# Kernel optimization log

Measured on AMD Instinct MI355X. Metric: run time of the kernel, lower is better.

The kernel has to match this reference:

```python
import jax, jax.numpy as jnp
import numpy as np

NUM_EXPERT = 8
IN_FEAT = 512
OUT_FEAT = 512
TOKENS = 16384


def setup_inputs() -> dict:
    key = jax.random.key(0)
    k_inp, k_gate, k_w = jax.random.split(key, 3)
    inp = jax.random.uniform(k_inp, (TOKENS, IN_FEAT), dtype=jnp.float32)
    gate = jax.random.randint(k_gate, (TOKENS,), 0, NUM_EXPERT, dtype=jnp.int32)
    # nn.Linear-style init: U(-1/sqrt(in_feat), 1/sqrt(in_feat))
    bound = 1.0 / np.sqrt(IN_FEAT)
    weight = jax.random.uniform(
        k_w, (NUM_EXPERT, OUT_FEAT, IN_FEAT), dtype=jnp.float32,
        minval=-bound, maxval=bound)
    return {"inp": inp, "gate": gate, "weight": weight}


def reference(inp, gate, weight):
    # y_t = weight[gate[t]] @ x_t  (per-token expert-specific GEMM)
    # Implemented via one-hot dispatch to avoid gathering a [T, O, I] weight tensor.
    num_expert = weight.shape[0]
    dispatch = jax.nn.one_hot(gate, num_expert, dtype=inp.dtype)  # [T, E]
    xe = jnp.einsum('te,ti->eti', dispatch, inp)                  # [E, T, I]
    ye = jnp.einsum('eti,eoi->eto', xe, weight)                   # [E, T, O]
    out = jnp.einsum('eto,te->to', ye, dispatch)                  # [T, O]
    return out
```

## Files before the change

kernel.cpp:

```cpp
#include <hip/hip_runtime.h>
#include <hip/hip_bf16.h>

#define TOKENS 16384
#define NEXP 8
#define INF 512
#define OUTF 512

#define BM 64
#define BN 128
#define BK 64
#define NST (INF / BK)
#define MAXMT 40
#define EROWS (MAXMT * BM)

using f32x4 = __attribute__((ext_vector_type(4))) float;
using bfrag = __attribute__((ext_vector_type(8))) __bf16;
using s8v   = __attribute__((ext_vector_type(8))) short;

__device__ __forceinline__ short f2bf(float f) {
  union { float f; unsigned u; } v; v.f = f;
  unsigned r = v.u + 0x7fffu + ((v.u >> 16) & 1u);
  return (short)(r >> 16);
}

__device__ __forceinline__ void gload16(const void* g, void* l) {
  __builtin_amdgcn_global_load_lds(
      (const __attribute__((address_space(1))) unsigned int*)g,
      (__attribute__((address_space(3))) unsigned int*)l, 16, 0, 0);
}

__device__ __forceinline__ s8v pack8(float4 a, float4 b) {
  s8v p;
  p[0] = f2bf(a.x); p[1] = f2bf(a.y); p[2] = f2bf(a.z); p[3] = f2bf(a.w);
  p[4] = f2bf(b.x); p[5] = f2bf(b.y); p[6] = f2bf(b.z); p[7] = f2bf(b.w);
  return p;
}

__device__ __forceinline__ bfrag cvt8(f32x4 lo, f32x4 hi) {
  bfrag r;
  r[0] = (__bf16)lo[0]; r[1] = (__bf16)lo[1];
  r[2] = (__bf16)lo[2]; r[3] = (__bf16)lo[3];
  r[4] = (__bf16)hi[0]; r[5] = (__bf16)hi[1];
  r[6] = (__bf16)hi[2]; r[7] = (__bf16)hi[3];
  return r;
}

__global__ void k_zero(int* __restrict__ cursor) {
  if (threadIdx.x < NEXP) cursor[threadIdx.x] = 0;
}

__global__ void k_prep(const int* __restrict__ gate, int* __restrict__ cursor,
                       int* __restrict__ perm, const float* __restrict__ w,
                       s8v* __restrict__ wb) {
  __shared__ int lc[NEXP], lb[NEXP];
  const int bid = blockIdx.x, tid = threadIdx.x;
  if (bid < 64) {
    if (tid < NEXP) lc[tid] = 0;
    __syncthreads();
    int t = bid * 256 + tid;
    int e = gate[t];
    int ls = atomicAdd(&lc[e], 1);
    __syncthreads();
    if (tid < NEXP) lb[tid] = lc[tid] ? atomicAdd(&cursor[tid], lc[tid]) : 0;
    __syncthreads();
    perm[e * EROWS + lb[e] + ls] = t;
  } else {
    int idx = (bid - 64) * 256 + tid;
    const float4* src = (const float4*)w + (size_t)idx * 2;
    wb[idx] = pack8(src[0], src[1]);
  }
}

__global__ __launch_bounds__(256, 4)
void moe_gemm7(const float* __restrict__ inp, const short* __restrict__ wbf,
               const int* __restrict__ cursor, const int* __restrict__ perm,
               float* __restrict__ out) {
  const int bid = blockIdx.x;
  const int e  = bid & 7;
  const int nt = (bid >> 3) & 3;
  const int mt = bid >> 5;
  const int cnt = cursor[e];
  if (mt * BM >= cnt) return;
  const int m_valid = min(BM, cnt - mt * BM);
  const int* pb = perm + e * EROWS + mt * BM;

  __shared__ __align__(16) char Albs[BM * BK * 4];
  __shared__ __align__(16) char Blbs[BN * BK * 2];
  __shared__ int toks[BM];

  const int tid = threadIdx.x;
  if (tid < BM) toks[tid] = pb[(tid < m_valid) ? tid : 0];
  __syncthreads();

  const int lane = tid & 63;
  const int wid  = tid >> 6;
  const int wr = wid >> 1, wc = wid & 1;
  const int lr = lane & 15;
  const int lg = lane >> 4;

  const float* agp[4];
#pragma unroll
  for (int s = 0; s < 4; s++) {
    int row  = s * 16 + (tid >> 4);
    int clog = (tid & 15) ^ (row & 15);
    agp[s] = inp + (size_t)toks[row] * INF + clog * 4;
  }

  const short* Wbase = wbf + ((size_t)e * OUTF + (size_t)nt * BN) * INF;
  const short* bgp[4];
#pragma unroll
  for (int s = 0; s < 4; s++) {
    int row  = s * 32 + (tid >> 3);
    int clog = (tid & 7) ^ (row & 7);
    bgp[s] = Wbase + (size_t)row * INF + clog * 8;
  }

  f32x4 acc[2][4];
#pragma unroll
  for (int m = 0; m < 2; m++)
#pragma unroll
    for (int j = 0; j < 4; j++) acc[m][j] = (f32x4)0.0f;

  for (int t = 0; t < NST; t++) {
#pragma unroll
    for (int s = 0; s < 4; s++)
      gload16(agp[s] + t * BK, Albs + s * 4096 + tid * 16);
#pragma unroll
    for (int s = 0; s < 4; s++)
      gload16(bgp[s] + t * BK, Blbs + s * 4096 + tid * 16);
    __syncthreads();

#pragma unroll
    for (int ks = 0; ks < 2; ks++) {
      bfrag af[2], bv[4];
#pragma unroll
      for (int m = 0; m < 2; m++) {
        int row = wr * 32 + m * 16 + lr;
        int c0 = (ks * 8 + lg * 2) ^ (row & 15);
        int c1 = (ks * 8 + lg * 2 + 1) ^ (row & 15);
        f32x4 lo = *(const f32x4*)(Albs + row * 256 + c0 * 16);
        f32x4 hi = *(const f32x4*)(Albs + row * 256 + c1 * 16);
        af[m] = cvt8(lo, hi);
      }
#pragma unroll
      for (int j = 0; j < 4; j++) {
        int row = wc * 64 + j * 16 + lr;
        int c = (ks * 4 + lg) ^ (row & 7);
        bv[j] = *(const bfrag*)(Blbs + row * 128 + c * 16);
      }
#pragma unroll
      for (int m = 0; m < 2; m++)
#pragma unroll
        for (int j = 0; j < 4; j++)
          acc[m][j] = __builtin_amdgcn_mfma_f32_16x16x32_bf16(af[m], bv[j],
                                                              acc[m][j], 0, 0, 0);
    }
    if (t + 1 < NST) __syncthreads();
  }

#pragma unroll
  for (int m = 0; m < 2; m++) {
#pragma unroll
    for (int r = 0; r < 4; r++) {
      int rowE = wr * 32 + m * 16 + lg * 4 + r;
      if (rowE < m_valid) {
        float* orow = out + (size_t)toks[rowE] * OUTF + (size_t)nt * BN +
                      (size_t)wc * 64 + lr;
#pragma unroll
        for (int j = 0; j < 4; j++) orow[j * 16] = acc[m][j][r];
      }
    }
  }
}

extern "C" void kernel_launch(void* const* d_in, const int* in_sizes, int n_in,
                              void* d_out, int out_size, void* d_ws, size_t ws_size,
                              hipStream_t stream) {
  (void)in_sizes; (void)n_in; (void)out_size; (void)ws_size;
  const float* inp    = (const float*)d_in[0];
  const int*   gate   = (const int*)d_in[1];
  const float* weight = (const float*)d_in[2];
  float* out = (float*)d_out;

  char* ws = (char*)d_ws;
  int*   cursor = (int*)ws;
  int*   perm   = (int*)(ws + 4096);
  short* wbf    = (short*)(ws + (1 << 20));

  k_zero<<<1, 64, 0, stream>>>(cursor);
  k_prep<<<64 + (NEXP * OUTF * INF) / (256 * 8), 256, 0, stream>>>(
      gate, cursor, perm, weight, (s8v*)wbf);
  moe_gemm7<<<NEXP * 4 * MAXMT, 256, 0, stream>>>(inp, wbf, cursor, perm, out);
}
```

Baseline: 35.00 us.

## Triple-buffer LDS tiles with BK=32 to overlap async loads and MFMA

Shrinks the K tile to 32 and keeps three LDS buffers, prefetching two stages ahead with direct-to-LDS global loads. Partial vmcnt waits plus a raw s_barrier are meant to let compute on one stage overlap the loads of later stages, instead of the previous load-sync-compute-sync sequence on a single buffer. The swizzle patterns are reworked for the narrower tiles. Launch bounds drop to 3 blocks per CU because of the extra LDS, and the zeroing kernel is replaced by hipMemsetAsync. Correctness relies on the vmcnt(4) counts matching the four loads issued per stage.

```diff
diff --git a/kernel.cpp b/kernel.cpp
--- a/kernel.cpp
+++ b/kernel.cpp
@@ -8,7 +8,7 @@
 
 #define BM 64
 #define BN 128
-#define BK 64
+#define BK 32
 #define NST (INF / BK)
 #define MAXMT 40
 #define EROWS (MAXMT * BM)
@@ -43,10 +43,6 @@
   r[4] = (__bf16)hi[0]; r[5] = (__bf16)hi[1];
   r[6] = (__bf16)hi[2]; r[7] = (__bf16)hi[3];
   return r;
-}
-
-__global__ void k_zero(int* __restrict__ cursor) {
-  if (threadIdx.x < NEXP) cursor[threadIdx.x] = 0;
 }
 
 __global__ void k_prep(const int* __restrict__ gate, int* __restrict__ cursor,
@@ -71,8 +67,14 @@
   }
 }
 
-__global__ __launch_bounds__(256, 4)
-void moe_gemm7(const float* __restrict__ inp, const short* __restrict__ wbf,
+#define KBAR(N)                                                         \
+  asm volatile("s_waitcnt vmcnt(" #N ") lgkmcnt(0)" ::: "memory");      \
+  __builtin_amdgcn_sched_barrier(0);                                    \
+  __builtin_amdgcn_s_barrier();                                         \
+  __builtin_amdgcn_sched_barrier(0);
+
+__global__ __launch_bounds__(256, 3)
+void moe_gemm8(const float* __restrict__ inp, const short* __restrict__ wbf,
                const int* __restrict__ cursor, const int* __restrict__ perm,
                float* __restrict__ out) {
   const int bid = blockIdx.x;
@@ -84,8 +86,8 @@
   const int m_valid = min(BM, cnt - mt * BM);
   const int* pb = perm + e * EROWS + mt * BM;
 
-  __shared__ __align__(16) char Albs[BM * BK * 4];
-  __shared__ __align__(16) char Blbs[BN * BK * 2];
+  __shared__ __align__(16) char Albs[3][BM * BK * 4];
+  __shared__ __align__(16) char Blbs[3][BN * BK * 2];
   __shared__ int toks[BM];
 
   const int tid = threadIdx.x;
@@ -98,20 +100,20 @@
   const int lr = lane & 15;
   const int lg = lane >> 4;
 
-  const float* agp[4];
-#pragma unroll
-  for (int s = 0; s < 4; s++) {
-    int row  = s * 16 + (tid >> 4);
-    int clog = (tid & 15) ^ (row & 15);
-    agp[s] = inp + (size_t)toks[row] * INF + clog * 4;
-  }
-
-  const short* Wbase = wbf + ((size_t)e * OUTF + (size_t)nt * BN) * INF;
-  const short* bgp[4];
-#pragma unroll
-  for (int s = 0; s < 4; s++) {
+  const float* agp[2];
+#pragma unroll
+  for (int s = 0; s < 2; s++) {
     int row  = s * 32 + (tid >> 3);
     int clog = (tid & 7) ^ (row & 7);
+    agp[s] = inp + (size_t)toks[row] * INF + clog * 4;
+  }
+
+  const short* Wbase = wbf + ((size_t)e * OUTF + (size_t)nt * BN) * INF;
+  const short* bgp[2];
+#pragma unroll
+  for (int s = 0; s < 2; s++) {
+    int row  = s * 64 + (tid >> 2);
+    int clog = (tid & 3) ^ (row & 3);
     bgp[s] = Wbase + (size_t)row * INF + clog * 8;
   }
 
@@ -121,41 +123,51 @@
 #pragma unroll
     for (int j = 0; j < 4; j++) acc[m][j] = (f32x4)0.0f;
 
+#define DMA(t_)                                                               \
+  {                                                                           \
+    char* ab_ = (char*)Albs[(t_) % 3];                                        \
+    char* bb_ = (char*)Blbs[(t_) % 3];                                        \
+    gload16(agp[0] + (t_) * BK, ab_ + tid * 16);                              \
+    gload16(agp[1] + (t_) * BK, ab_ + 4096 + tid * 16);                       \
+    gload16(bgp[0] + (t_) * BK, bb_ + tid * 16);                              \
+    gload16(bgp[1] + (t_) * BK, bb_ + 4096 + tid * 16);                       \
+  }
+#define COMP(t_)                                                              \
+  {                                                                           \
+    const char* ab_ = (const char*)Albs[(t_) % 3];                            \
+    const char* bb_ = (const char*)Blbs[(t_) % 3];                            \
+    bfrag af[2], bv[4];                                                       \
+    _Pragma("unroll") for (int m = 0; m < 2; m++) {                           \
+      int row = wr * 32 + m * 16 + lr;                                        \
+      int c0 = (lg * 2) ^ (row & 7), c1 = (lg * 2 + 1) ^ (row & 7);           \
+      f32x4 lo = *(const f32x4*)(ab_ + row * 128 + c0 * 16);                  \
+      f32x4 hi = *(const f32x4*)(ab_ + row * 128 + c1 * 16);                  \
+      af[m] = cvt8(lo, hi);                                                   \
+    }                                                                         \
+    _Pragma("unroll") for (int j = 0; j < 4; j++) {                           \
+      int row = wc * 64 + j * 16 + lr;                                        \
+      int c = lg ^ (row & 3);                                                 \
+      bv[j] = *(const bfrag*)(bb_ + row * 64 + c * 16);                       \
+    }                                                                         \
+    _Pragma("unroll") for (int m = 0; m < 2; m++)                             \
+      _Pragma("unroll") for (int j = 0; j < 4; j++)                           \
+          acc[m][j] = __builtin_amdgcn_mfma_f32_16x16x32_bf16(                \
+              af[m], bv[j], acc[m][j], 0, 0, 0);                              \
+  }
+
+  DMA(0);
+  DMA(1);
+  KBAR(4)
+
+#pragma unroll
   for (int t = 0; t < NST; t++) {
-#pragma unroll
-    for (int s = 0; s < 4; s++)
-      gload16(agp[s] + t * BK, Albs + s * 4096 + tid * 16);
-#pragma unroll
-    for (int s = 0; s < 4; s++)
-      gload16(bgp[s] + t * BK, Blbs + s * 4096 + tid * 16);
-    __syncthreads();
-
-#pragma unroll
-    for (int ks = 0; ks < 2; ks++) {
-      bfrag af[2], bv[4];
-#pragma unroll
-      for (int m = 0; m < 2; m++) {
-        int row = wr * 32 + m * 16 + lr;
-        int c0 = (ks * 8 + lg * 2) ^ (row & 15);
-        int c1 = (ks * 8 + lg * 2 + 1) ^ (row & 15);
-        f32x4 lo = *(const f32x4*)(Albs + row * 256 + c0 * 16);
-        f32x4 hi = *(const f32x4*)(Albs + row * 256 + c1 * 16);
-        af[m] = cvt8(lo, hi);
-      }
-#pragma unroll
-      for (int j = 0; j < 4; j++) {
-        int row = wc * 64 + j * 16 + lr;
-        int c = (ks * 4 + lg) ^ (row & 7);
-        bv[j] = *(const bfrag*)(Blbs + row * 128 + c * 16);
-      }
-#pragma unroll
-      for (int m = 0; m < 2; m++)
-#pragma unroll
-        for (int j = 0; j < 4; j++)
-          acc[m][j] = __builtin_amdgcn_mfma_f32_16x16x32_bf16(af[m], bv[j],
-                                                              acc[m][j], 0, 0, 0);
+    if (t + 2 < NST) DMA(t + 2);
+    COMP(t);
+    if (t + 2 < NST) {
+      KBAR(4)
+    } else if (t + 1 < NST) {
+      KBAR(0)
     }
-    if (t + 1 < NST) __syncthreads();
   }
 
 #pragma unroll
@@ -171,6 +183,8 @@
       }
     }
   }
+#undef DMA
+#undef COMP
 }
 
 extern "C" void kernel_launch(void* const* d_in, const int* in_sizes, int n_in,
@@ -187,8 +201,8 @@
   int*   perm   = (int*)(ws + 4096);
   short* wbf    = (short*)(ws + (1 << 20));
 
-  k_zero<<<1, 64, 0, stream>>>(cursor);
+  hipMemsetAsync(cursor, 0, 64, stream);
   k_prep<<<64 + (NEXP * OUTF * INF) / (256 * 8), 256, 0, stream>>>(
       gate, cursor, perm, weight, (s8v*)wbf);
-  moe_gemm7<<<NEXP * 4 * MAXMT, 256, 0, stream>>>(inp, wbf, cursor, perm, out);
-}
+  moe_gemm8<<<NEXP * 4 * MAXMT, 256, 0, stream>>>(inp, wbf, cursor, perm, out);
+}
```

Result: slower. 37.93 us (+8.4%).
